# Performance work log

Hardware: AMD Instinct MI355X
Metric: run time of the kernel (lower is better)

## Reference

```python
import jax, jax.numpy as jnp
import numpy as np

B, T, D, H, O = 32, 2048, 256, 512, 256


def setup_inputs() -> dict:
    key = jax.random.key(0)
    ks = jax.random.split(key, 8)
    s = lambda k, shp, fan: jax.random.normal(k, shp, dtype=jnp.float32) / np.sqrt(fan)
    return {
        "x": jax.random.normal(ks[0], (B, T, D), dtype=jnp.float32),
        "h0": jax.random.normal(ks[1], (1, B, H), dtype=jnp.float32),
        "W_ih": s(ks[2], (H, D), D),
        "W_hh": s(ks[3], (H, H), H),
        "b_ih": jnp.zeros((H,), jnp.float32),
        "b_hh": jnp.zeros((H,), jnp.float32),
        "W_lin": s(ks[4], (O, H), H),
        "b_lin": jnp.zeros((O,), jnp.float32),
    }


def reference(x, h0, W_ih, W_hh, b_ih, b_hh, W_lin, b_lin):
    # rnn_act == 'linear' branch: h_t = x_t @ W_ih^T + h_{t-1} @ W_hh^T + b_ih + b_hh
    h_init = h0[0]  # [B, H]
    # Precompute the input contribution for all timesteps at once: [B, T, H]
    xw = jnp.einsum("btd,hd->bth", x, W_ih) + (b_ih + b_hh)

    def step(h, xw_t):  # xw_t: [B, H]
        h_new = xw_t + h @ W_hh.T
        return h_new, h_new

    # scan over time axis
    _, z_t = jax.lax.scan(step, h_init, jnp.swapaxes(xw, 0, 1))  # [T, B, H]
    z = jnp.swapaxes(z_t, 0, 1)  # [B, T, H]

    logits = jnp.einsum("bth,oh->bto", z, W_lin) + b_lin
    out = jax.nn.softmax(logits, axis=2)
    return out, z
```

## Files before the change

kernel.cpp:

```cpp
#include <hip/hip_runtime.h>
#include <math.h>

#define B_ 32
#define T_ 2048
#define D_ 256
#define H_ 512
#define O_ 256
#define S_CH 8
#define C_CH 256

typedef short bf16x8 __attribute__((ext_vector_type(8)));
typedef float f32x4  __attribute__((ext_vector_type(4)));

#define NTL(p)     __builtin_nontemporal_load(p)

__device__ __forceinline__ unsigned short f2bf_rne(float x) {
    unsigned int u = __builtin_bit_cast(unsigned int, x);
    unsigned int r = (u + 0x7fffu + ((u >> 16) & 1u)) >> 16;
    return (unsigned short)r;
}
__device__ __forceinline__ float bf2f(unsigned short h) {
    unsigned int u = ((unsigned int)h) << 16;
    return __builtin_bit_cast(float, u);
}

#define MFMA16(a, b, c) __builtin_amdgcn_mfma_f32_16x16x32_bf16((a), (b), (c), 0, 0, 0)

__device__ __forceinline__ void split_frag(const float* p, bf16x8& hi, bf16x8& lo) {
    f32x4 a = *(const f32x4*)p;
    f32x4 b = *(const f32x4*)(p + 4);
#pragma unroll
    for (int i = 0; i < 4; i++) {
        unsigned short h = f2bf_rne(a[i]);
        hi[i] = (short)h; lo[i] = (short)f2bf_rne(a[i] - bf2f(h));
        unsigned short h2 = f2bf_rne(b[i]);
        hi[4 + i] = (short)h2; lo[4 + i] = (short)f2bf_rne(b[i] - bf2f(h2));
    }
}
__device__ __forceinline__ void split_frag_nt(const float* p, bf16x8& hi, bf16x8& lo) {
    f32x4 a = NTL((const f32x4*)p);
    f32x4 b = NTL((const f32x4*)(p + 4));
#pragma unroll
    for (int i = 0; i < 4; i++) {
        unsigned short h = f2bf_rne(a[i]);
        hi[i] = (short)h; lo[i] = (short)f2bf_rne(a[i] - bf2f(h));
        unsigned short h2 = f2bf_rne(b[i]);
        hi[4 + i] = (short)h2; lo[4 + i] = (short)f2bf_rne(b[i] - bf2f(h2));
    }
}

__device__ __forceinline__ size_t wpack_off(int n, int k, int KB) {
    int n16 = n >> 4, l15 = n & 15;
    int kb = k >> 5, lhi = (k >> 3) & 3, j = k & 7;
    return (((size_t)(n16 * KB + kb) * 4 + lhi) * 16 + l15) * 8 + j;
}

__device__ __forceinline__ int hfrag_off(int m, int n) {
    int m16 = m >> 4, l15m = m & 15;
    int kb = n >> 5, lhi = (n >> 3) & 3, j = n & 7;
    return (((m16 * 16 + kb) * 4 + lhi) * 16 + l15m) * 8 + j;
}

__global__ void k_pack(const float* __restrict__ in, unsigned short* __restrict__ hi,
                       unsigned short* __restrict__ lo, int total, int kshift) {
    int i = blockIdx.x * 256 + threadIdx.x;
    if (i < total) {
        int n = i >> kshift;
        int k = i & ((1 << kshift) - 1);
        float v = in[i];
        unsigned short h = f2bf_rne(v);
        size_t o = wpack_off(n, k, 1 << (kshift - 5));
        hi[o] = h;
        lo[o] = f2bf_rne(v - bf2f(h));
    }
}

__global__ __launch_bounds__(256) void k_mul(const float* __restrict__ A,
                                             const float* __restrict__ Bm,
                                             float* __restrict__ Out) {
    __shared__ float As[32][33];
    __shared__ float Bs[32][33];
    int tx = threadIdx.x & 15, ty = threadIdx.x >> 4;
    int j0 = blockIdx.x * 32, i0 = blockIdx.y * 32;
    float a00 = 0.f, a01 = 0.f, a10 = 0.f, a11 = 0.f;
    int r  = threadIdx.x >> 3;
    int c4 = (threadIdx.x & 7) * 4;
    for (int kb = 0; kb < H_ / 32; kb++) {
        f32x4 va = *(const f32x4*)(A + (size_t)(i0 + r) * H_ + kb * 32 + c4);
        f32x4 vb = *(const f32x4*)(Bm + (size_t)(kb * 32 + r) * H_ + j0 + c4);
        __syncthreads();
        As[r][c4 + 0] = va[0]; As[r][c4 + 1] = va[1]; As[r][c4 + 2] = va[2]; As[r][c4 + 3] = va[3];
        Bs[r][c4 + 0] = vb[0]; Bs[r][c4 + 1] = vb[1]; Bs[r][c4 + 2] = vb[2]; Bs[r][c4 + 3] = vb[3];
        __syncthreads();
#pragma unroll
        for (int k = 0; k < 32; k++) {
            float b0 = Bs[k][tx * 2], b1 = Bs[k][tx * 2 + 1];
            float a0 = As[ty * 2][k], a1 = As[ty * 2 + 1][k];
            a00 += a0 * b0; a01 += a0 * b1; a10 += a1 * b0; a11 += a1 * b1;
        }
    }
    Out[(size_t)(i0 + ty * 2) * H_ + j0 + tx * 2]     = a00;
    Out[(size_t)(i0 + ty * 2) * H_ + j0 + tx * 2 + 1] = a01;
    Out[(size_t)(i0 + ty * 2 + 1) * H_ + j0 + tx * 2]     = a10;
    Out[(size_t)(i0 + ty * 2 + 1) * H_ + j0 + tx * 2 + 1] = a11;
}

__global__ void k_seed(const float* __restrict__ h0, const float* __restrict__ zb,
                       float* __restrict__ Va) {
    int i = blockIdx.x * 256 + threadIdx.x;
    int c = i >> 14;
    int bn = i & 16383;
    int b = bn >> 9, n = bn & 511;
    Va[i] = (c == 0) ? h0[bn] : zb[((size_t)b * T_ + (c * S_CH - 1)) * H_ + n];
}

__global__ __launch_bounds__(512) void k_scan2(const float* __restrict__ Vin,
                                               const unsigned short* __restrict__ Qp_hi,
                                               const unsigned short* __restrict__ Qp_lo,
                                               float* __restrict__ Vout, int s) {
    __shared__ __attribute__((aligned(16))) unsigned short hA[16384];
    __shared__ __attribute__((aligned(16))) unsigned short lA[16384];
    int c = blockIdx.x;
    int w = threadIdx.x >> 6;
    int lane = threadIdx.x & 63;
    int l15 = lane & 15, lhi = lane >> 4;

    if (c < s) {
        size_t base = (size_t)c * B_ * H_;
        for (int i = threadIdx.x * 4; i < B_ * H_; i += 2048) {
            f32x4 v = *(const f32x4*)(Vin + base + i);
            *(f32x4*)(Vout + base + i) = v;
        }
        return;
    }

    size_t src = (size_t)(c - s) * B_ * H_;
    for (int i = threadIdx.x; i < 16384; i += 512) {
        float v = Vin[src + i];
        int m = i >> 9, n = i & 511;
        unsigned short hi = f2bf_rne(v);
        int o = hfrag_off(m, n);
        hA[o] = hi;
        lA[o] = f2bf_rne(v - bf2f(hi));
    }
    __syncthreads();

    size_t dst = (size_t)c * B_ * H_;
    float ad[2][4][4];
#pragma unroll
    for (int mt = 0; mt < 2; mt++)
#pragma unroll
        for (int nt = 0; nt < 4; nt++) {
            int n = w * 64 + nt * 16 + l15;
#pragma unroll
            for (int r = 0; r < 4; r++) {
                int m = mt * 16 + lhi * 4 + r;
                ad[mt][nt][r] = Vin[dst + (size_t)m * H_ + n];
            }
        }

    f32x4 acc[2][4];
#pragma unroll
    for (int mt = 0; mt < 2; mt++)
#pragma unroll
        for (int nt = 0; nt < 4; nt++) acc[mt][nt] = (f32x4){0.f, 0.f, 0.f, 0.f};

    for (int kb = 0; kb < 16; kb++) {
        bf16x8 ah0 = *(const bf16x8*)&hA[(kb << 9) + lane * 8];
        bf16x8 ah1 = *(const bf16x8*)&hA[((16 + kb) << 9) + lane * 8];
        bf16x8 al0 = *(const bf16x8*)&lA[(kb << 9) + lane * 8];
        bf16x8 al1 = *(const bf16x8*)&lA[((16 + kb) << 9) + lane * 8];
#pragma unroll
        for (int nt = 0; nt < 4; nt++) {
            size_t wb = (((size_t)(w * 4 + nt) * 16 + kb) << 9) + lane * 8;
            bf16x8 bh = *(const bf16x8*)(Qp_hi + wb);
            bf16x8 bl = *(const bf16x8*)(Qp_lo + wb);
            acc[0][nt] = MFMA16(ah0, bh, acc[0][nt]);
            acc[0][nt] = MFMA16(al0, bh, acc[0][nt]);
            acc[0][nt] = MFMA16(ah0, bl, acc[0][nt]);
            acc[1][nt] = MFMA16(ah1, bh, acc[1][nt]);
            acc[1][nt] = MFMA16(al1, bh, acc[1][nt]);
            acc[1][nt] = MFMA16(ah1, bl, acc[1][nt]);
        }
    }
#pragma unroll
    for (int mt = 0; mt < 2; mt++)
#pragma unroll
        for (int nt = 0; nt < 4; nt++) {
            int n = w * 64 + nt * 16 + l15;
#pragma unroll
            for (int r = 0; r < 4; r++) {
                int m = mt * 16 + lhi * 4 + r;
                Vout[dst + (size_t)m * H_ + n] = acc[mt][nt][r] + ad[mt][nt][r];
            }
        }
}

__global__ __launch_bounds__(512) void k_xw(const float* __restrict__ x,
                                            const unsigned short* __restrict__ Wp_hi,
                                            const unsigned short* __restrict__ Wp_lo,
                                            const float* __restrict__ bih,
                                            const float* __restrict__ bhh,
                                            float* __restrict__ zb) {
    int b  = blockIdx.y;
    int t0 = blockIdx.x * 64;
    int w    = threadIdx.x >> 6;
    int lane = threadIdx.x & 63;
    int l15 = lane & 15, lhi = lane >> 4;
    int nb = w * 64;

    f32x4 acc[4][4];
    for (int mt = 0; mt < 4; mt++)
        for (int nt = 0; nt < 4; nt++)
            acc[mt][nt] = (f32x4){0.f, 0.f, 0.f, 0.f};

    const float* xb = x + (size_t)b * T_ * D_;
    for (int kb = 0; kb < D_ / 32; kb++) {
        int kofs = kb * 32 + lhi * 8;
        bf16x8 ah[4], al[4];
#pragma unroll
        for (int mt = 0; mt < 4; mt++) {
            int t = t0 + mt * 16 + l15;
            split_frag_nt(xb + (size_t)t * D_ + kofs, ah[mt], al[mt]);
        }
#pragma unroll
        for (int nt = 0; nt < 4; nt++) {
            size_t wb = (((size_t)(w * 4 + nt) * 8 + kb) << 9) + lane * 8;
            bf16x8 bh = *(const bf16x8*)(Wp_hi + wb);
            bf16x8 bl = *(const bf16x8*)(Wp_lo + wb);
#pragma unroll
            for (int mt = 0; mt < 4; mt++) {
                acc[mt][nt] = MFMA16(ah[mt], bh, acc[mt][nt]);
                acc[mt][nt] = MFMA16(al[mt], bh, acc[mt][nt]);
                acc[mt][nt] = MFMA16(ah[mt], bl, acc[mt][nt]);
            }
        }
    }
#pragma unroll
    for (int nt = 0; nt < 4; nt++) {
        int n = nb + nt * 16 + l15;
        float bias = bih[n] + bhh[n];
#pragma unroll
        for (int mt = 0; mt < 4; mt++) {
#pragma unroll
            for (int r = 0; r < 4; r++) {
                int t = t0 + mt * 16 + lhi * 4 + r;
                zb[((size_t)b * T_ + t) * H_ + n] = acc[mt][nt][r] + bias;
            }
        }
    }
}

__global__ __launch_bounds__(512) void k_phase1(const unsigned short* __restrict__ Wp_hi,
                                                const unsigned short* __restrict__ Wp_lo,
                                                float* __restrict__ zb) {
    __shared__ __attribute__((aligned(16))) unsigned short hA[16384];
    __shared__ __attribute__((aligned(16))) unsigned short lA[16384];
    int c = blockIdx.x;
    int w = threadIdx.x >> 6;
    int lane = threadIdx.x & 63;
    int l15 = lane & 15, lhi = lane >> 4;

    for (int i = threadIdx.x; i < 16384; i += 512) { hA[i] = 0; lA[i] = 0; }
    __syncthreads();

    for (int j = 0; j < S_CH; j++) {
        int t = c * S_CH + j;
        float xw[2][4][4];
#pragma unroll
        for (int mt = 0; mt < 2; mt++)
#pragma unroll
            for (int nt = 0; nt < 4; nt++) {
                int n = w * 64 + nt * 16 + l15;
#pragma unroll
                for (int r = 0; r < 4; r++) {
                    int b = mt * 16 + lhi * 4 + r;
                    xw[mt][nt][r] = zb[((size_t)b * T_ + t) * H_ + n];
                }
            }
        f32x4 acc[2][4];
#pragma unroll
        for (int mt = 0; mt < 2; mt++)
#pragma unroll
            for (int nt = 0; nt < 4; nt++) acc[mt][nt] = (f32x4){0.f, 0.f, 0.f, 0.f};
        if (j > 0) {
            for (int kb = 0; kb < 16; kb++) {
                bf16x8 ah0 = *(const bf16x8*)&hA[(kb << 9) + lane * 8];
                bf16x8 ah1 = *(const bf16x8*)&hA[((16 + kb) << 9) + lane * 8];
                bf16x8 al0 = *(const bf16x8*)&lA[(kb << 9) + lane * 8];
                bf16x8 al1 = *(const bf16x8*)&lA[((16 + kb) << 9) + lane * 8];
#pragma unroll
                for (int nt = 0; nt < 4; nt++) {
                    size_t wb = (((size_t)(w * 4 + nt) * 16 + kb) << 9) + lane * 8;
                    bf16x8 bh = *(const bf16x8*)(Wp_hi + wb);
                    bf16x8 bl = *(const bf16x8*)(Wp_lo + wb);
                    acc[0][nt] = MFMA16(ah0, bh, acc[0][nt]);
                    acc[0][nt] = MFMA16(al0, bh, acc[0][nt]);
                    acc[0][nt] = MFMA16(ah0, bl, acc[0][nt]);
                    acc[1][nt] = MFMA16(ah1, bh, acc[1][nt]);
                    acc[1][nt] = MFMA16(al1, bh, acc[1][nt]);
                    acc[1][nt] = MFMA16(ah1, bl, acc[1][nt]);
                }
            }
        }
        __syncthreads();
#pragma unroll
        for (int mt = 0; mt < 2; mt++) {
#pragma unroll
            for (int nt = 0; nt < 4; nt++) {
                int n = w * 64 + nt * 16 + l15;
#pragma unroll
                for (int r = 0; r < 4; r++) {
                    int b = mt * 16 + lhi * 4 + r;
                    float v = acc[mt][nt][r] + xw[mt][nt][r];
                    zb[((size_t)b * T_ + t) * H_ + n] = v;
                    unsigned short hi = f2bf_rne(v);
                    int o = hfrag_off(b, n);
                    hA[o] = hi;
                    lA[o] = f2bf_rne(v - bf2f(hi));
                }
            }
        }
        __syncthreads();
    }
}

__global__ __launch_bounds__(512) void k_carry(const float* __restrict__ Hin,
                                               const unsigned short* __restrict__ Pp_hi,
                                               const unsigned short* __restrict__ Pp_lo,
                                               float* __restrict__ zb) {
    int bid = blockIdx.x;
    int swz = (bid & 7) * 128 + (bid >> 3);
    int npanel = swz >> 6;
    int mtile  = swz & 63;
    int w = threadIdx.x >> 6, lane = threadIdx.x & 63;
    int l15 = lane & 15, lhi = lane >> 4;
    int wm = w >> 2, wn = w & 3;
    int m0 = mtile * 128 + wm * 64;
    int n16base = npanel * 16 + wn * 4;

    f32x4 acc[4][4];
#pragma unroll
    for (int mt = 0; mt < 4; mt++)
#pragma unroll
        for (int nt = 0; nt < 4; nt++) acc[mt][nt] = (f32x4){0.f, 0.f, 0.f, 0.f};

    for (int kb = 0; kb < 16; kb++) {
        int kofs = kb * 32 + lhi * 8;
        bf16x8 ah[4], al[4];
#pragma unroll
        for (int mt = 0; mt < 4; mt++)
            split_frag(Hin + (size_t)(m0 + mt * 16 + l15) * H_ + kofs, ah[mt], al[mt]);
#pragma unroll
        for (int nt = 0; nt < 4; nt++) {
            size_t wb = (((size_t)(n16base + nt) * 16 + kb) << 9) + lane * 8;
            bf16x8 bh = *(const bf16x8*)(Pp_hi + wb);
            bf16x8 bl = *(const bf16x8*)(Pp_lo + wb);
#pragma unroll
            for (int mt = 0; mt < 4; mt++) {
                acc[mt][nt] = MFMA16(ah[mt], bh, acc[mt][nt]);
                acc[mt][nt] = MFMA16(al[mt], bh, acc[mt][nt]);
                acc[mt][nt] = MFMA16(ah[mt], bl, acc[mt][nt]);
            }
        }
    }
#pragma unroll
    for (int nt = 0; nt < 4; nt++) {
        int col = (n16base + nt) * 16 + l15;
        int j = col >> 9, n = col & 511;
#pragma unroll
        for (int mt = 0; mt < 4; mt++) {
#pragma unroll
            for (int r = 0; r < 4; r++) {
                int m = m0 + mt * 16 + lhi * 4 + r;
                int c = m >> 5, b = m & 31;
                size_t zi = ((size_t)b * T_ + (c * S_CH + j)) * H_ + n;
                zb[zi] += acc[mt][nt][r];
            }
        }
    }
}

__global__ __launch_bounds__(256) void k_logits(const float* __restrict__ zq,
                                                const unsigned short* __restrict__ Wp_hi,
                                                const float* __restrict__ blin,
                                                float* __restrict__ out) {
    size_t row0 = (size_t)blockIdx.x * 64;
    int w = threadIdx.x >> 6, lane = threadIdx.x & 63;
    int l15 = lane & 15, lhi = lane >> 4;

    f32x4 acc[16];
#pragma unroll
    for (int nt = 0; nt < 16; nt++) acc[nt] = (f32x4){0.f, 0.f, 0.f, 0.f};

    const float* arow = zq + (row0 + (size_t)w * 16 + l15) * H_;
    for (int kb = 0; kb < 16; kb++) {
        int kofs = kb * 32 + lhi * 8;
        bf16x8 ah, al;
        split_frag_nt(arow + kofs, ah, al);
#pragma unroll
        for (int nt = 0; nt < 16; nt++) {
            size_t wb = (((size_t)nt * 16 + kb) << 9) + lane * 8;
            bf16x8 bh = *(const bf16x8*)(Wp_hi + wb);
            acc[nt] = MFMA16(ah, bh, acc[nt]);
            acc[nt] = MFMA16(al, bh, acc[nt]);
        }
    }
#pragma unroll
    for (int nt = 0; nt < 16; nt++) {
        float bb = blin[nt * 16 + l15];
#pragma unroll
        for (int r = 0; r < 4; r++) acc[nt][r] += bb;
    }
    float rmax[4], rinv[4];
#pragma unroll
    for (int r = 0; r < 4; r++) {
        float mx = -INFINITY;
#pragma unroll
        for (int nt = 0; nt < 16; nt++) mx = fmaxf(mx, acc[nt][r]);
        for (int s = 1; s < 16; s <<= 1) mx = fmaxf(mx, __shfl_xor(mx, s));
        float sum = 0.f;
#pragma unroll
        for (int nt = 0; nt < 16; nt++) sum += __expf(acc[nt][r] - mx);
        for (int s = 1; s < 16; s <<= 1) sum += __shfl_xor(sum, s);
        rmax[r] = mx;
        rinv[r] = 1.f / sum;
    }
#pragma unroll
    for (int nt = 0; nt < 16; nt++) {
#pragma unroll
        for (int r = 0; r < 4; r++) {
            float e = __expf(acc[nt][r] - rmax[r]) * rinv[r];
            size_t row = row0 + (size_t)w * 16 + lhi * 4 + r;
            out[row * O_ + nt * 16 + l15] = e;
        }
    }
}

extern "C" void kernel_launch(void* const* d_in, const int* in_sizes, int n_in,
                              void* d_out, int out_size, void* d_ws, size_t ws_size,
                              hipStream_t stream) {
    const float* x    = (const float*)d_in[0];
    const float* h0   = (const float*)d_in[1];
    const float* Wih  = (const float*)d_in[2];
    const float* Whh  = (const float*)d_in[3];
    const float* bih  = (const float*)d_in[4];
    const float* bhh  = (const float*)d_in[5];
    const float* Wlin = (const float*)d_in[6];
    const float* blin = (const float*)d_in[7];

    float* out  = (float*)d_out;
    float* zout = out + (size_t)B_ * T_ * O_;

    float* ws = (float*)d_ws;
    float* M[14];
    for (int i = 0; i < 14; i++) M[i] = ws + (size_t)i * H_ * H_;
    unsigned short* Whh_hi = (unsigned short*)(ws + (size_t)14 * H_ * H_);
    unsigned short* Whh_lo = Whh_hi + (size_t)H_ * H_;
    unsigned short* Wih_hi = Whh_lo + (size_t)H_ * H_;
    unsigned short* Wih_lo = Wih_hi + (size_t)H_ * D_;
    unsigned short* Wlin_hi = Wih_lo + (size_t)H_ * D_;
    unsigned short* Wlin_lo = Wlin_hi + (size_t)O_ * H_;
    (void)Wlin_lo;

    float* Va = out;
    float* Vb = out + (size_t)C_CH * B_ * H_;
    unsigned short* Pp_hi = (unsigned short*)((char*)d_out + (size_t)32 * 1024 * 1024);
    unsigned short* Pp_lo = Pp_hi + (size_t)8 * H_ * H_;
    unsigned short* Qp_hi = Pp_lo + (size_t)8 * H_ * H_;
    unsigned short* Qp_lo = Qp_hi + (size_t)8 * H_ * H_;

    k_pack<<<dim3((H_ * H_) / 256), 256, 0, stream>>>(Whh, Whh_hi, Whh_lo, H_ * H_, 9);
    k_pack<<<dim3((H_ * D_) / 256), 256, 0, stream>>>(Wih, Wih_hi, Wih_lo, H_ * D_, 8);
    k_pack<<<dim3((O_ * H_) / 256), 256, 0, stream>>>(Wlin, Wlin_hi, Wlin_lo, O_ * H_, 9);

    dim3 g16(16, 16);
    k_mul<<<g16, 256, 0, stream>>>(Whh, Whh, M[0]);
    k_mul<<<g16, 256, 0, stream>>>(Whh, M[0], M[1]);
    k_mul<<<g16, 256, 0, stream>>>(M[0], M[0], M[2]);
    k_mul<<<g16, 256, 0, stream>>>(Whh, M[2], M[3]);
    k_mul<<<g16, 256, 0, stream>>>(M[0], M[2], M[4]);
    k_mul<<<g16, 256, 0, stream>>>(M[1], M[2], M[5]);
    k_mul<<<g16, 256, 0, stream>>>(M[2], M[2], M[6]);
    for (int i = 7; i < 14; i++)
        k_mul<<<g16, 256, 0, stream>>>(M[i - 1], M[i - 1], M[i]);

    k_pack<<<dim3((H_ * H_) / 256), 256, 0, stream>>>(Whh, Pp_hi, Pp_lo, H_ * H_, 9);
    for (int j = 2; j <= 8; j++)
        k_pack<<<dim3((H_ * H_) / 256), 256, 0, stream>>>(
            M[j - 2], Pp_hi + (size_t)(j - 1) * H_ * H_, Pp_lo + (size_t)(j - 1) * H_ * H_,
            H_ * H_, 9);
    for (int l = 0; l < 8; l++)
        k_pack<<<dim3((H_ * H_) / 256), 256, 0, stream>>>(
            M[6 + l], Qp_hi + (size_t)l * H_ * H_, Qp_lo + (size_t)l * H_ * H_, H_ * H_, 9);

    k_xw<<<dim3(T_ / 64, B_), 512, 0, stream>>>(x, Wih_hi, Wih_lo, bih, bhh, zout);

    k_phase1<<<dim3(C_CH), 512, 0, stream>>>(Whh_hi, Whh_lo, zout);

    k_seed<<<dim3((C_CH * B_ * H_) / 256), 256, 0, stream>>>(h0, zout, Va);
    {
        float* vin = Va;
        float* vout = Vb;
        int s = 1;
        for (int l = 0; l < 8; l++) {
            k_scan2<<<dim3(C_CH), 512, 0, stream>>>(
                vin, Qp_hi + (size_t)l * H_ * H_, Qp_lo + (size_t)l * H_ * H_, vout, s);
            float* tmp = vin; vin = vout; vout = tmp;
            s <<= 1;
        }
    }

    k_carry<<<dim3(1024), 512, 0, stream>>>(Va, Pp_hi, Pp_lo, zout);

    k_logits<<<dim3((B_ * T_) / 64), 256, 0, stream>>>(zout, Wlin_hi, blin, out);
}
```

Measured before the change: 1.603 ms.

## Fuse bf16 split packing into matrix-power kernels and double scan/phase1 block size

The hi/lo bf16 packing of the W_hh powers is fused into the k_mul epilogue, which removes fifteen separate k_pack launches and their re-reads of the fp32 matrices. k_scan2 and k_phase1 now run 1024 threads per block with 16 waves each covering 32 output columns instead of 8 waves covering 64, giving more parallelism on the latency-bound scan steps. The zero-init of the shared h buffer in k_phase1 is dropped because the j==0 step never reads it. The trade-off is more waves contending for LDS and barriers, plus scattered 16-bit stores in the k_mul epilogue.

```diff
diff --git a/kernel.cpp b/kernel.cpp
--- a/kernel.cpp
+++ b/kernel.cpp
@@ -77,7 +77,11 @@
 
 __global__ __launch_bounds__(256) void k_mul(const float* __restrict__ A,
                                              const float* __restrict__ Bm,
-                                             float* __restrict__ Out) {
+                                             float* __restrict__ Out,
+                                             unsigned short* __restrict__ d1h,
+                                             unsigned short* __restrict__ d1l,
+                                             unsigned short* __restrict__ d2h,
+                                             unsigned short* __restrict__ d2l) {
     __shared__ float As[32][33];
     __shared__ float Bs[32][33];
     int tx = threadIdx.x & 15, ty = threadIdx.x >> 4;
@@ -99,10 +103,18 @@
             a00 += a0 * b0; a01 += a0 * b1; a10 += a1 * b0; a11 += a1 * b1;
         }
     }
-    Out[(size_t)(i0 + ty * 2) * H_ + j0 + tx * 2]     = a00;
-    Out[(size_t)(i0 + ty * 2) * H_ + j0 + tx * 2 + 1] = a01;
-    Out[(size_t)(i0 + ty * 2 + 1) * H_ + j0 + tx * 2]     = a10;
-    Out[(size_t)(i0 + ty * 2 + 1) * H_ + j0 + tx * 2 + 1] = a11;
+    float vals[4] = {a00, a01, a10, a11};
+#pragma unroll
+    for (int q = 0; q < 4; q++) {
+        int n = i0 + ty * 2 + (q >> 1);
+        int k = j0 + tx * 2 + (q & 1);
+        Out[(size_t)n * H_ + k] = vals[q];
+        unsigned short h = f2bf_rne(vals[q]);
+        unsigned short l = f2bf_rne(vals[q] - bf2f(h));
+        size_t o = wpack_off(n, k, 16);
+        if (d1h) { d1h[o] = h; d1l[o] = l; }
+        if (d2h) { d2h[o] = h; d2l[o] = l; }
+    }
 }
 
 __global__ void k_seed(const float* __restrict__ h0, const float* __restrict__ zb,
@@ -114,10 +126,10 @@
     Va[i] = (c == 0) ? h0[bn] : zb[((size_t)b * T_ + (c * S_CH - 1)) * H_ + n];
 }
 
-__global__ __launch_bounds__(512) void k_scan2(const float* __restrict__ Vin,
-                                               const unsigned short* __restrict__ Qp_hi,
-                                               const unsigned short* __restrict__ Qp_lo,
-                                               float* __restrict__ Vout, int s) {
+__global__ __launch_bounds__(1024) void k_scan2(const float* __restrict__ Vin,
+                                                const unsigned short* __restrict__ Qp_hi,
+                                                const unsigned short* __restrict__ Qp_lo,
+                                                float* __restrict__ Vout, int s) {
     __shared__ __attribute__((aligned(16))) unsigned short hA[16384];
     __shared__ __attribute__((aligned(16))) unsigned short lA[16384];
     int c = blockIdx.x;
@@ -127,7 +139,7 @@
 
     if (c < s) {
         size_t base = (size_t)c * B_ * H_;
-        for (int i = threadIdx.x * 4; i < B_ * H_; i += 2048) {
+        for (int i = threadIdx.x * 4; i < B_ * H_; i += 4096) {
             f32x4 v = *(const f32x4*)(Vin + base + i);
             *(f32x4*)(Vout + base + i) = v;
         }
@@ -135,7 +147,7 @@
     }
 
     size_t src = (size_t)(c - s) * B_ * H_;
-    for (int i = threadIdx.x; i < 16384; i += 512) {
+    for (int i = threadIdx.x; i < 16384; i += 1024) {
         float v = Vin[src + i];
         int m = i >> 9, n = i & 511;
         unsigned short hi = f2bf_rne(v);
@@ -146,12 +158,12 @@
     __syncthreads();
 
     size_t dst = (size_t)c * B_ * H_;
-    float ad[2][4][4];
+    float ad[2][2][4];
 #pragma unroll
     for (int mt = 0; mt < 2; mt++)
 #pragma unroll
-        for (int nt = 0; nt < 4; nt++) {
-            int n = w * 64 + nt * 16 + l15;
+        for (int nt = 0; nt < 2; nt++) {
+            int n = w * 32 + nt * 16 + l15;
 #pragma unroll
             for (int r = 0; r < 4; r++) {
                 int m = mt * 16 + lhi * 4 + r;
@@ -159,11 +171,11 @@
             }
         }
 
-    f32x4 acc[2][4];
+    f32x4 acc[2][2];
 #pragma unroll
     for (int mt = 0; mt < 2; mt++)
 #pragma unroll
-        for (int nt = 0; nt < 4; nt++) acc[mt][nt] = (f32x4){0.f, 0.f, 0.f, 0.f};
+        for (int nt = 0; nt < 2; nt++) acc[mt][nt] = (f32x4){0.f, 0.f, 0.f, 0.f};
 
     for (int kb = 0; kb < 16; kb++) {
         bf16x8 ah0 = *(const bf16x8*)&hA[(kb << 9) + lane * 8];
@@ -171,8 +183,8 @@
         bf16x8 al0 = *(const bf16x8*)&lA[(kb << 9) + lane * 8];
         bf16x8 al1 = *(const bf16x8*)&lA[((16 + kb) << 9) + lane * 8];
 #pragma unroll
-        for (int nt = 0; nt < 4; nt++) {
-            size_t wb = (((size_t)(w * 4 + nt) * 16 + kb) << 9) + lane * 8;
+        for (int nt = 0; nt < 2; nt++) {
+            size_t wb = (((size_t)(w * 2 + nt) * 16 + kb) << 9) + lane * 8;
             bf16x8 bh = *(const bf16x8*)(Qp_hi + wb);
             bf16x8 bl = *(const bf16x8*)(Qp_lo + wb);
             acc[0][nt] = MFMA16(ah0, bh, acc[0][nt]);
@@ -186,8 +198,8 @@
 #pragma unroll
     for (int mt = 0; mt < 2; mt++)
 #pragma unroll
-        for (int nt = 0; nt < 4; nt++) {
-            int n = w * 64 + nt * 16 + l15;
+        for (int nt = 0; nt < 2; nt++) {
+            int n = w * 32 + nt * 16 + l15;
 #pragma unroll
             for (int r = 0; r < 4; r++) {
                 int m = mt * 16 + lhi * 4 + r;
@@ -251,9 +263,9 @@
     }
 }
 
-__global__ __launch_bounds__(512) void k_phase1(const unsigned short* __restrict__ Wp_hi,
-                                                const unsigned short* __restrict__ Wp_lo,
-                                                float* __restrict__ zb) {
+__global__ __launch_bounds__(1024) void k_phase1(const unsigned short* __restrict__ Wp_hi,
+                                                 const unsigned short* __restrict__ Wp_lo,
+                                                 float* __restrict__ zb) {
     __shared__ __attribute__((aligned(16))) unsigned short hA[16384];
     __shared__ __attribute__((aligned(16))) unsigned short lA[16384];
     int c = blockIdx.x;
@@ -261,28 +273,25 @@
     int lane = threadIdx.x & 63;
     int l15 = lane & 15, lhi = lane >> 4;
 
-    for (int i = threadIdx.x; i < 16384; i += 512) { hA[i] = 0; lA[i] = 0; }
-    __syncthreads();
-
     for (int j = 0; j < S_CH; j++) {
         int t = c * S_CH + j;
-        float xw[2][4][4];
+        float xw[2][2][4];
 #pragma unroll
         for (int mt = 0; mt < 2; mt++)
 #pragma unroll
-            for (int nt = 0; nt < 4; nt++) {
-                int n = w * 64 + nt * 16 + l15;
+            for (int nt = 0; nt < 2; nt++) {
+                int n = w * 32 + nt * 16 + l15;
 #pragma unroll
                 for (int r = 0; r < 4; r++) {
                     int b = mt * 16 + lhi * 4 + r;
                     xw[mt][nt][r] = zb[((size_t)b * T_ + t) * H_ + n];
                 }
             }
-        f32x4 acc[2][4];
+        f32x4 acc[2][2];
 #pragma unroll
         for (int mt = 0; mt < 2; mt++)
 #pragma unroll
-            for (int nt = 0; nt < 4; nt++) acc[mt][nt] = (f32x4){0.f, 0.f, 0.f, 0.f};
+            for (int nt = 0; nt < 2; nt++) acc[mt][nt] = (f32x4){0.f, 0.f, 0.f, 0.f};
         if (j > 0) {
             for (int kb = 0; kb < 16; kb++) {
                 bf16x8 ah0 = *(const bf16x8*)&hA[(kb << 9) + lane * 8];
@@ -290,8 +299,8 @@
                 bf16x8 al0 = *(const bf16x8*)&lA[(kb << 9) + lane * 8];
                 bf16x8 al1 = *(const bf16x8*)&lA[((16 + kb) << 9) + lane * 8];
 #pragma unroll
-                for (int nt = 0; nt < 4; nt++) {
-                    size_t wb = (((size_t)(w * 4 + nt) * 16 + kb) << 9) + lane * 8;
+                for (int nt = 0; nt < 2; nt++) {
+                    size_t wb = (((size_t)(w * 2 + nt) * 16 + kb) << 9) + lane * 8;
                     bf16x8 bh = *(const bf16x8*)(Wp_hi + wb);
                     bf16x8 bl = *(const bf16x8*)(Wp_lo + wb);
                     acc[0][nt] = MFMA16(ah0, bh, acc[0][nt]);
@@ -307,8 +316,8 @@
 #pragma unroll
         for (int mt = 0; mt < 2; mt++) {
 #pragma unroll
-            for (int nt = 0; nt < 4; nt++) {
-                int n = w * 64 + nt * 16 + l15;
+            for (int nt = 0; nt < 2; nt++) {
+                int n = w * 32 + nt * 16 + l15;
 #pragma unroll
                 for (int r = 0; r < 4; r++) {
                     int b = mt * 16 + lhi * 4 + r;
@@ -471,32 +480,35 @@
     unsigned short* Qp_lo = Qp_hi + (size_t)8 * H_ * H_;
 
     k_pack<<<dim3((H_ * H_) / 256), 256, 0, stream>>>(Whh, Whh_hi, Whh_lo, H_ * H_, 9);
+    k_pack<<<dim3((H_ * H_) / 256), 256, 0, stream>>>(Whh, Pp_hi, Pp_lo, H_ * H_, 9);
     k_pack<<<dim3((H_ * D_) / 256), 256, 0, stream>>>(Wih, Wih_hi, Wih_lo, H_ * D_, 8);
     k_pack<<<dim3((O_ * H_) / 256), 256, 0, stream>>>(Wlin, Wlin_hi, Wlin_lo, O_ * H_, 9);
 
     dim3 g16(16, 16);
-    k_mul<<<g16, 256, 0, stream>>>(Whh, Whh, M[0]);
-    k_mul<<<g16, 256, 0, stream>>>(Whh, M[0], M[1]);
-    k_mul<<<g16, 256, 0, stream>>>(M[0], M[0], M[2]);
-    k_mul<<<g16, 256, 0, stream>>>(Whh, M[2], M[3]);
-    k_mul<<<g16, 256, 0, stream>>>(M[0], M[2], M[4]);
-    k_mul<<<g16, 256, 0, stream>>>(M[1], M[2], M[5]);
-    k_mul<<<g16, 256, 0, stream>>>(M[2], M[2], M[6]);
+    size_t HH = (size_t)H_ * H_;
+    unsigned short* nul = nullptr;
+#define PPH(s) (Pp_hi + (size_t)(s) * HH)
+#define PPL(s) (Pp_lo + (size_t)(s) * HH)
+#define QPH(s) (Qp_hi + (size_t)(s) * HH)
+#define QPL(s) (Qp_lo + (size_t)(s) * HH)
+    k_mul<<<g16, 256, 0, stream>>>(Whh, Whh, M[0], PPH(1), PPL(1), nul, nul);
+    k_mul<<<g16, 256, 0, stream>>>(Whh, M[0], M[1], PPH(2), PPL(2), nul, nul);
+    k_mul<<<g16, 256, 0, stream>>>(M[0], M[0], M[2], PPH(3), PPL(3), nul, nul);
+    k_mul<<<g16, 256, 0, stream>>>(Whh, M[2], M[3], PPH(4), PPL(4), nul, nul);
+    k_mul<<<g16, 256, 0, stream>>>(M[0], M[2], M[4], PPH(5), PPL(5), nul, nul);
+    k_mul<<<g16, 256, 0, stream>>>(M[1], M[2], M[5], PPH(6), PPL(6), nul, nul);
+    k_mul<<<g16, 256, 0, stream>>>(M[2], M[2], M[6], PPH(7), PPL(7), QPH(0), QPL(0));
     for (int i = 7; i < 14; i++)
-        k_mul<<<g16, 256, 0, stream>>>(M[i - 1], M[i - 1], M[i]);
-
-    k_pack<<<dim3((H_ * H_) / 256), 256, 0, stream>>>(Whh, Pp_hi, Pp_lo, H_ * H_, 9);
-    for (int j = 2; j <= 8; j++)
-        k_pack<<<dim3((H_ * H_) / 256), 256, 0, stream>>>(
-            M[j - 2], Pp_hi + (size_t)(j - 1) * H_ * H_, Pp_lo + (size_t)(j - 1) * H_ * H_,
-            H_ * H_, 9);
-    for (int l = 0; l < 8; l++)
-        k_pack<<<dim3((H_ * H_) / 256), 256, 0, stream>>>(
-            M[6 + l], Qp_hi + (size_t)l * H_ * H_, Qp_lo + (size_t)l * H_ * H_, H_ * H_, 9);
+        k_mul<<<g16, 256, 0, stream>>>(M[i - 1], M[i - 1], M[i],
+                                       QPH(i - 6), QPL(i - 6), nul, nul);
+#undef PPH
+#undef PPL
+#undef QPH
+#undef QPL
 
     k_xw<<<dim3(T_ / 64, B_), 512, 0, stream>>>(x, Wih_hi, Wih_lo, bih, bhh, zout);
 
-    k_phase1<<<dim3(C_CH), 512, 0, stream>>>(Whh_hi, Whh_lo, zout);
+    k_phase1<<<dim3(C_CH), 1024, 0, stream>>>(Whh_hi, Whh_lo, zout);
 
     k_seed<<<dim3((C_CH * B_ * H_) / 256), 256, 0, stream>>>(h0, zout, Va);
     {
@@ -504,8 +516,8 @@
         float* vout = Vb;
         int s = 1;
         for (int l = 0; l < 8; l++) {
-            k_scan2<<<dim3(C_CH), 512, 0, stream>>>(
-                vin, Qp_hi + (size_t)l * H_ * H_, Qp_lo + (size_t)l * H_ * H_, vout, s);
+            k_scan2<<<dim3(C_CH), 1024, 0, stream>>>(
+                vin, Qp_hi + (size_t)l * HH, Qp_lo + (size_t)l * HH, vout, s);
             float* tmp = vin; vin = vout; vout = tmp;
             s <<= 1;
         }
```

Result: faster. 1.353 ms (-15.6%).
